# Kernel tuning notes

Measured on AMD Instinct MI355X. Metric: run time of the kernel, lower is better.

The kernel has to match this reference:

```python
import jax, jax.numpy as jnp
import numpy as np

B, D, Q, U = 4096, 512, 16384, 256  # batch, feat dim, CQ size, unique pids per batch
OIM_SCALAR = 30.0
IGNORE = -1


def _normalize(x):
    # F.normalize(dim=-1): divide by L2 norm clamped to eps
    n = jnp.maximum(jnp.linalg.norm(x, axis=-1, keepdims=True), 1e-12)
    return x / n


def setup_inputs() -> dict:
    key = jax.random.key(0)
    k1, k2, k3 = jax.random.split(key, 3)
    inputs = jax.random.normal(k1, (B, D), dtype=jnp.float32)
    # exactly U unique pids, each repeated B//U times, shuffled
    labels = jax.random.permutation(k2, jnp.arange(B, dtype=jnp.int32) % U)
    emb_cq = jax.random.normal(k3, (Q, D), dtype=jnp.float32)
    emb_cq = _normalize(emb_cq)  # queue stores normalized embeddings
    # unique queue labels; slice overlaps batch pids -> exercises the c==1 branch
    label_cq = jnp.arange(Q, dtype=jnp.int32) + 1000
    label_cq = label_cq.at[5000:5000 + U].set(jnp.arange(U, dtype=jnp.int32))
    age_cq = jnp.ones((Q,), dtype=jnp.int32)
    return {"inputs": inputs, "labels": labels, "emb_cq": emb_cq,
            "label_cq": label_cq, "age_cq": age_cq, "header_cq": 0}


def reference(inputs, labels, emb_cq, label_cq, age_cq, header_cq):
    # ---- per-pid masked mean (torch.unique loop, vectorized) ----
    uniq = jnp.unique(labels, size=U)                      # sorted unique pids [U]
    m_u = (uniq[:, None] == labels[None, :]).astype(inputs.dtype)  # [U,B]
    uniq_emb = (m_u @ inputs) / m_u.sum(axis=1, keepdims=True)     # [U,D]

    inputs_n = _normalize(inputs)
    uniq_emb_n = jax.lax.stop_gradient(_normalize(uniq_emb))  # queue write is under no_grad

    # ---- circular queue update (sequential, data-dependent) ----
    age_cq = age_cq + (label_cq != IGNORE).astype(age_cq.dtype)

    def step(carry, xy):
        emb, lab, age, h = carry
        x, y = xy
        m = lab == y
        c = m.any()
        i = jnp.argmax(m)          # existing slot for pid y (if any)
        emb = emb.at[h].set(x)
        lab = lab.at[h].set(y)
        age = age.at[h].set(1)
        inval = c & (i != h)       # invalidate stale slot
        lab = lab.at[i].set(jnp.where(inval, IGNORE, lab[i]))
        age = age.at[i].set(jnp.where(inval, 0, age[i]))
        return (emb, lab, age, (h + 1) % Q), None

    h0 = jnp.asarray(header_cq, dtype=jnp.int32)
    (emb_cq, label_cq, age_cq, _), _ = jax.lax.scan(
        step, (emb_cq, label_cq, age_cq, h0), (uniq_emb_n, uniq))
    emb_cq = jax.lax.stop_gradient(emb_cq)  # buffer: no grad through the queue

    # ---- cosine-sim cross-entropy over valid queue entries ----
    good = label_cq != IGNORE                               # [Q]
    # each batch pid matches exactly one good queue slot
    xe = jnp.argmax((labels[:, None] == label_cq[None, :]) & good[None, :], axis=1)
    logits = OIM_SCALAR * (inputs_n @ emb_cq.T)             # [B,Q]
    logits = jnp.where(good[None, :], logits, -jnp.inf)     # mask == compacting emb_cq[good]
    logp = jax.nn.log_softmax(logits, axis=1)
    loss = -jnp.mean(logp[jnp.arange(B), xe])               # sum(xe_i)/B
    return loss
```

## Files before the change

kernel.cpp:

```cpp
#include <hip/hip_runtime.h>
#include <hip/hip_bf16.h>

#define Bn 4096
#define Dn 512
#define Qn 16384
#define Un 256
#define OIM 30.0f


typedef int i32x4 __attribute__((ext_vector_type(4)));

__device__ __forceinline__ int clamp8(float v, float qs) {
    int q = __float2int_rn(v * qs);
    return max(-127, min(127, q));
}

__global__ void prep_kernel(const float* __restrict__ inputs, const int* __restrict__ labels,
                            const float* __restrict__ emb_cq, const int* __restrict__ label_cq,
                            const int* __restrict__ header,
                            char* __restrict__ inA8, char* __restrict__ embQ8,
                            float* __restrict__ invA, float* __restrict__ invB,
                            float* __restrict__ goodf, float* __restrict__ rowsum,
                            float* __restrict__ out) {
    __shared__ float wred[4];
    __shared__ float wmax[4];
    __shared__ int lidx[64];
    __shared__ int lcnt;
    int blk = blockIdx.x;
    int tid = threadIdx.x;
    float2 o;
    bool isA;
    int drow;
    if (blk == 0 && tid == 0) out[0] = 0.f;
    if (blk < Bn) {
        if (tid == 0) rowsum[blk] = 0.f;
        float2 v = ((const float2*)(inputs + (size_t)blk * Dn))[tid];
        float ss = v.x * v.x + v.y * v.y;
        for (int d = 1; d < 64; d <<= 1) ss += __shfl_xor(ss, d, 64);
        if ((tid & 63) == 0) wred[tid >> 6] = ss;
        __syncthreads();
        float sc = 1.0f / fmaxf(sqrtf(wred[0] + wred[1] + wred[2] + wred[3]), 1e-12f);
        o.x = v.x * sc; o.y = v.y * sc;
        isA = true; drow = blk;
    } else {
        int j = blk - Bn;
        int h0 = header[0];
        int t = j - h0; if (t < 0) t += Qn;
        if (t < Un) {
            if (tid == 0) lcnt = 0;
            __syncthreads();
            for (int b = tid; b < Bn; b += 256)
                if (labels[b] == t) { int s = atomicAdd(&lcnt, 1); if (s < 64) lidx[s] = b; }
            __syncthreads();
            int c = lcnt; if (c > 64) c = 64;
            float2 acc = {0.f, 0.f};
            for (int s = 0; s < c; ++s) {
                float2 x = ((const float2*)(inputs + (size_t)lidx[s] * Dn))[tid];
                acc.x += x.x; acc.y += x.y;
            }
            float inv = 1.0f / (float)(c > 0 ? c : 1);
            acc.x *= inv; acc.y *= inv;
            float ss = acc.x * acc.x + acc.y * acc.y;
            for (int d = 1; d < 64; d <<= 1) ss += __shfl_xor(ss, d, 64);
            if ((tid & 63) == 0) wred[tid >> 6] = ss;
            __syncthreads();
            float sc = 1.0f / fmaxf(sqrtf(wred[0] + wred[1] + wred[2] + wred[3]), 1e-12f);
            o.x = acc.x * sc; o.y = acc.y * sc;
        } else {
            o = ((const float2*)(emb_cq + (size_t)j * Dn))[tid];
        }
        if (tid == 0) {
            int vl = label_cq[j];
            int fin = (vl >= 0 && vl < Un) ? -1 : vl;
            if (t < Un) fin = t;
            goodf[j] = (fin != -1) ? 1.0f : 0.0f;
        }
        isA = false; drow = blk - Bn;
    }
    float am = fmaxf(fabsf(o.x), fabsf(o.y));
    for (int d = 1; d < 64; d <<= 1) am = fmaxf(am, __shfl_xor(am, d, 64));
    if ((tid & 63) == 0) wmax[tid >> 6] = am;
    __syncthreads();
    float m = fmaxf(fmaxf(fmaxf(wmax[0], wmax[1]), fmaxf(wmax[2], wmax[3])), 1e-12f);
    float qs = 127.0f / m;
    char2 pc;
    pc.x = (char)clamp8(o.x, qs);
    pc.y = (char)clamp8(o.y, qs);
    int kb = tid * 2;
    size_t addr = (size_t)(drow >> 4) * 8192 + (size_t)(kb >> 4) * 256
                + (drow & 15) * 16 + (kb & 15);
    if (isA) {
        *(char2*)(inA8 + addr) = pc;
        if (tid == 0) invA[drow] = m / 127.0f;
    } else {
        *(char2*)(embQ8 + addr) = pc;
        if (tid == 0) invB[drow] = m / 127.0f;
    }
}

__global__ __launch_bounds__(256, 4) void gemm_kernel(
    const char* __restrict__ inA8,
    const char* __restrict__ embQ8,
    const float* __restrict__ invA,
    const float* __restrict__ invB,
    const float* __restrict__ goodf,
    const int* __restrict__ labels,
    const int* __restrict__ header,
    float* __restrict__ rowsum,
    float* __restrict__ target)
{
    const float LOG2E = 1.4426950408889634f;
    const float LN2   = 0.6931471805599453f;
    __shared__ float rsl[128];
    __shared__ int tgtc[128];
    __shared__ float sAl[128];
    __shared__ float2 sBL[128];
    int tid = threadIdx.x;
    int lane = tid & 63, w = tid >> 6;
    int wm = w >> 1, wn = w & 1;
    int lid = blockIdx.y * gridDim.x + blockIdx.x;
    int xcd = lid & 7, pos = lid >> 3;
    int n0 = (xcd * 16 + (pos & 15)) * 128;
    int m0 = (pos >> 4) * 128;
    if (tid < 128) {
        rsl[tid] = 0.f;
        int tc = header[0] + labels[m0 + tid];
        if (tc >= Qn) tc -= Qn;
        tgtc[tid] = tc;
        sAl[tid] = invA[m0 + tid];
        float2 sb;
        sb.x = invB[n0 + tid];
        sb.y = (goodf[n0 + tid] != 0.f) ? 0.f : -10000.f;
        sBL[tid] = sb;
    }
    __syncthreads();
    i32x4 acc[4][4] = {};
    const char* Ap[4];
    const char* Bp[4];
    #pragma unroll
    for (int i = 0; i < 4; ++i) {
        Ap[i] = inA8  + (size_t)((m0 >> 4) + wm * 4 + i) * 8192 + lane * 16;
        Bp[i] = embQ8 + (size_t)((n0 >> 4) + wn * 4 + i) * 8192 + lane * 16;
    }
    i32x4 a0[4], a1[4], b0[4], b1[4];
    #pragma unroll
    for (int i = 0; i < 4; ++i) {
        a0[i] = *(const i32x4*)(Ap[i]);
        b0[i] = *(const i32x4*)(Bp[i]);
    }
    #pragma unroll
    for (int t = 0; t < 8; ++t) {
        if (t < 7) {
            if (t & 1) {
                #pragma unroll
                for (int i = 0; i < 4; ++i) {
                    a0[i] = *(const i32x4*)(Ap[i] + (t + 1) * 1024);
                    b0[i] = *(const i32x4*)(Bp[i] + (t + 1) * 1024);
                }
            } else {
                #pragma unroll
                for (int i = 0; i < 4; ++i) {
                    a1[i] = *(const i32x4*)(Ap[i] + (t + 1) * 1024);
                    b1[i] = *(const i32x4*)(Bp[i] + (t + 1) * 1024);
                }
            }
        }
        if (t & 1) {
            #pragma unroll
            for (int i = 0; i < 4; ++i)
                #pragma unroll
                for (int j = 0; j < 4; ++j)
                    acc[i][j] = __builtin_amdgcn_mfma_i32_16x16x64_i8(b1[j], a1[i], acc[i][j], 0, 0, 0);
        } else {
            #pragma unroll
            for (int i = 0; i < 4; ++i)
                #pragma unroll
                for (int j = 0; j < 4; ++j)
                    acc[i][j] = __builtin_amdgcn_mfma_i32_16x16x64_i8(b0[j], a0[i], acc[i][j], 0, 0, 0);
        }
    }
    int q = lane >> 4;
    int bl = lane & 15;
    float2 sbv[16];
    #pragma unroll
    for (int j = 0; j < 4; ++j)
        #pragma unroll
        for (int r = 0; r < 4; ++r)
            sbv[j * 4 + r] = sBL[wn * 64 + j * 16 + q * 4 + r];
    #pragma unroll
    for (int i = 0; i < 4; ++i) {
        int rowl = wm * 64 + i * 16 + bl;
        float fA = (OIM * LOG2E) * sAl[rowl];
        int tc = tgtc[rowl];
        float s = 0.f;
        #pragma unroll
        for (int j = 0; j < 4; ++j) {
            #pragma unroll
            for (int r = 0; r < 4; ++r) {
                int qloc = wn * 64 + j * 16 + q * 4 + r;
                float2 sb = sbv[j * 4 + r];
                float v2 = fA * sb.x * (float)acc[i][j][r] + sb.y;
                s += __builtin_amdgcn_exp2f(v2);
                if (tc == n0 + qloc) target[m0 + rowl] = v2 * LN2;
            }
        }
        s += __shfl_xor(s, 16, 64);
        s += __shfl_xor(s, 32, 64);
        if (q == 0) atomicAdd(&rsl[rowl], s);
    }
    __syncthreads();
    if (tid < 128) atomicAdd(&rowsum[m0 + tid], rsl[tid]);
}

__global__ void loss_kernel(const float* __restrict__ rowsum, const float* __restrict__ target,
                            float* __restrict__ out) {
    __shared__ float red[4];
    int tid = threadIdx.x;
    int b = blockIdx.x * 256 + tid;
    float s = logf(rowsum[b]) - target[b];
    #pragma unroll
    for (int d = 1; d < 64; d <<= 1) s += __shfl_xor(s, d, 64);
    if ((tid & 63) == 0) red[tid >> 6] = s;
    __syncthreads();
    if (tid == 0)
        atomicAdd(out, (red[0] + red[1] + red[2] + red[3]) * (1.0f / (float)Bn));
}

extern "C" void kernel_launch(void* const* d_in, const int* in_sizes, int n_in,
                              void* d_out, int out_size, void* d_ws, size_t ws_size,
                              hipStream_t stream) {
    const float* inputs   = (const float*)d_in[0];
    const int*   labels   = (const int*)d_in[1];
    const float* emb_cq   = (const float*)d_in[2];
    const int*   label_cq = (const int*)d_in[3];
    const int*   header   = (const int*)d_in[5];

    char* ws = (char*)d_ws;
    size_t off = 0;
    auto alloc = [&](size_t bytes) { char* p = ws + off; off += (bytes + 255) & ~(size_t)255; return p; };
    char*  inA8   = (char*)alloc((size_t)Bn * Dn);
    char*  embQ8  = (char*)alloc((size_t)Qn * Dn);
    float* invA   = (float*)alloc(Bn * 4);
    float* invB   = (float*)alloc(Qn * 4);
    float* goodf  = (float*)alloc(Qn * 4);
    float* rowsum = (float*)alloc(Bn * 4);
    float* target = (float*)alloc(Bn * 4);

    hipLaunchKernelGGL(prep_kernel, dim3(Bn + Qn), dim3(256), 0, stream,
                       inputs, labels, emb_cq, label_cq, header,
                       inA8, embQ8, invA, invB, goodf, rowsum, (float*)d_out);
    hipLaunchKernelGGL(gemm_kernel, dim3(Qn / 128, Bn / 128), dim3(256), 0, stream,
                       inA8, embQ8, invA, invB, goodf, labels, header, rowsum, target);
    hipLaunchKernelGGL(loss_kernel, dim3(Bn / 256), dim3(256), 0, stream,
                       rowsum, target, (float*)d_out);
}
```

Baseline: 181.0 us.

## Stage queue-embedding tiles through LDS with async global-to-LDS copies

The int8 queue embeddings are now written row-major instead of in the pre-tiled MFMA layout. Inside the GEMM, B tiles are streamed per wave into a double-buffered LDS region with global_load_lds async copies, using a swizzled layout to avoid bank conflicts. A operands are still loaded straight into registers, and explicit vmcnt waits plus sched barriers overlap the copies with the MFMAs. This is meant to hide global-load latency and lower register pressure for B, at the cost of extra LDS use and hand-tuned wait counts that may be fragile.

```diff
diff --git a/kernel.cpp b/kernel.cpp
--- a/kernel.cpp
+++ b/kernel.cpp
@@ -9,6 +9,11 @@
 
 
 typedef int i32x4 __attribute__((ext_vector_type(4)));
+
+__device__ __forceinline__ void async_copy16(const int4* g, int4* l) {
+    __builtin_amdgcn_global_load_lds((const __attribute__((address_space(1))) void*)g,
+                                     (__attribute__((address_space(3))) void*)l, 16, 0, 0);
+}
 
 __device__ __forceinline__ int clamp8(float v, float qs) {
     int q = __float2int_rn(v * qs);
@@ -86,17 +91,53 @@
     char2 pc;
     pc.x = (char)clamp8(o.x, qs);
     pc.y = (char)clamp8(o.y, qs);
-    int kb = tid * 2;
-    size_t addr = (size_t)(drow >> 4) * 8192 + (size_t)(kb >> 4) * 256
-                + (drow & 15) * 16 + (kb & 15);
     if (isA) {
+        int kb = tid * 2;
+        size_t addr = (size_t)(drow >> 4) * 8192 + (size_t)(kb >> 4) * 256
+                    + (drow & 15) * 16 + (kb & 15);
         *(char2*)(inA8 + addr) = pc;
         if (tid == 0) invA[drow] = m / 127.0f;
     } else {
-        *(char2*)(embQ8 + addr) = pc;
+        *(char2*)(embQ8 + (size_t)drow * Dn + tid * 2) = pc;
         if (tid == 0) invB[drow] = m / 127.0f;
     }
 }
+
+#define STAGEW(T, SLOT) do {                                                  \
+    _Pragma("unroll")                                                         \
+    for (int u = 0; u < 4; ++u)                                               \
+        async_copy16(&Bg[goffW[u] + (T) * 4],                                 \
+                     &Bs4[w * 512 + (SLOT) * 256 + u * 64]);                  \
+} while (0)
+
+#define BODY(T, ACUR, ANXT) do {                                              \
+    __builtin_amdgcn_sched_barrier(0);                                        \
+    if ((T) < 7) asm volatile("s_waitcnt vmcnt(4)");                          \
+    else         asm volatile("s_waitcnt vmcnt(0)");                          \
+    __builtin_amdgcn_sched_barrier(0);                                        \
+    i32x4 bfr[4];                                                             \
+    _Pragma("unroll")                                                         \
+    for (int j = 0; j < 4; ++j)                                               \
+        bfr[j] = *(const i32x4*)(Bs + w * 8192 + ((T) & 1) * 4096 + offBW[j]);\
+    asm volatile("s_waitcnt lgkmcnt(0)");                                     \
+    __builtin_amdgcn_sched_barrier(0);                                        \
+    if ((T) < 7) {                                                            \
+        _Pragma("unroll")                                                     \
+        for (int i = 0; i < 4; ++i)                                           \
+            ANXT[i] = *(const i32x4*)(Ap[i] + ((T) + 1) * 1024);              \
+    }                                                                         \
+    __builtin_amdgcn_sched_barrier(0);                                        \
+    if ((T) < 6) STAGEW((T) + 2, (T) & 1);                                    \
+    __builtin_amdgcn_sched_barrier(0);                                        \
+    __builtin_amdgcn_s_setprio(1);                                            \
+    _Pragma("unroll")                                                         \
+    for (int i = 0; i < 4; ++i)                                               \
+        _Pragma("unroll")                                                     \
+        for (int j = 0; j < 4; ++j)                                           \
+            acc[i][j] = __builtin_amdgcn_mfma_i32_16x16x64_i8(                \
+                bfr[j], ACUR[i], acc[i][j], 0, 0, 0);                         \
+    __builtin_amdgcn_s_setprio(0);                                            \
+} while (0)
 
 __global__ __launch_bounds__(256, 4) void gemm_kernel(
     const char* __restrict__ inA8,
@@ -111,6 +152,7 @@
 {
     const float LOG2E = 1.4426950408889634f;
     const float LN2   = 0.6931471805599453f;
+    __shared__ char Bs[4 * 2 * 4096];
     __shared__ float rsl[128];
     __shared__ int tgtc[128];
     __shared__ float sAl[128];
@@ -135,52 +177,37 @@
     }
     __syncthreads();
     i32x4 acc[4][4] = {};
-    const char* Ap[4];
-    const char* Bp[4];
-    #pragma unroll
-    for (int i = 0; i < 4; ++i) {
-        Ap[i] = inA8  + (size_t)((m0 >> 4) + wm * 4 + i) * 8192 + lane * 16;
-        Bp[i] = embQ8 + (size_t)((n0 >> 4) + wn * 4 + i) * 8192 + lane * 16;
-    }
-    i32x4 a0[4], a1[4], b0[4], b1[4];
-    #pragma unroll
-    for (int i = 0; i < 4; ++i) {
-        a0[i] = *(const i32x4*)(Ap[i]);
-        b0[i] = *(const i32x4*)(Bp[i]);
-    }
-    #pragma unroll
-    for (int t = 0; t < 8; ++t) {
-        if (t < 7) {
-            if (t & 1) {
-                #pragma unroll
-                for (int i = 0; i < 4; ++i) {
-                    a0[i] = *(const i32x4*)(Ap[i] + (t + 1) * 1024);
-                    b0[i] = *(const i32x4*)(Bp[i] + (t + 1) * 1024);
-                }
-            } else {
-                #pragma unroll
-                for (int i = 0; i < 4; ++i) {
-                    a1[i] = *(const i32x4*)(Ap[i] + (t + 1) * 1024);
-                    b1[i] = *(const i32x4*)(Bp[i] + (t + 1) * 1024);
-                }
-            }
-        }
-        if (t & 1) {
-            #pragma unroll
-            for (int i = 0; i < 4; ++i)
-                #pragma unroll
-                for (int j = 0; j < 4; ++j)
-                    acc[i][j] = __builtin_amdgcn_mfma_i32_16x16x64_i8(b1[j], a1[i], acc[i][j], 0, 0, 0);
-        } else {
-            #pragma unroll
-            for (int i = 0; i < 4; ++i)
-                #pragma unroll
-                for (int j = 0; j < 4; ++j)
-                    acc[i][j] = __builtin_amdgcn_mfma_i32_16x16x64_i8(b0[j], a0[i], acc[i][j], 0, 0, 0);
-        }
-    }
+    const int4* Bg = (const int4*)(embQ8 + (size_t)n0 * Dn);
+    int4* Bs4 = (int4*)Bs;
+    int csw = ((lane & 3) - ((lane >> 3) & 3)) & 3;
+    int goffW[4];
+    #pragma unroll
+    for (int u = 0; u < 4; ++u)
+        goffW[u] = (wn * 64 + u * 16 + (lane >> 2)) * 32 + csw;
     int q = lane >> 4;
     int bl = lane & 15;
+    int offBW[4];
+    #pragma unroll
+    for (int j = 0; j < 4; ++j)
+        offBW[j] = (j * 16 + bl) * 64 + (((q + (bl >> 1)) & 3) << 4);
+    const char* Ap[4];
+    #pragma unroll
+    for (int i = 0; i < 4; ++i)
+        Ap[i] = inA8 + (size_t)((m0 >> 4) + wm * 4 + i) * 8192 + lane * 16;
+    i32x4 a0[4], a1[4];
+    #pragma unroll
+    for (int i = 0; i < 4; ++i) a0[i] = *(const i32x4*)(Ap[i]);
+    __builtin_amdgcn_sched_barrier(0);
+    STAGEW(0, 0);
+    STAGEW(1, 1);
+    BODY(0, a0, a1);
+    BODY(1, a1, a0);
+    BODY(2, a0, a1);
+    BODY(3, a1, a0);
+    BODY(4, a0, a1);
+    BODY(5, a1, a0);
+    BODY(6, a0, a1);
+    BODY(7, a1, a0);
     float2 sbv[16];
     #pragma unroll
     for (int j = 0; j < 4; ++j)
```

Measured after the change: 152.1 us. 16.0% less time.
